# Performance work log

Hardware: AMD Instinct MI355X
Metric: run time of the kernel (lower is better)

## Reference

```python
import jax, jax.numpy as jnp
import numpy as np

B, L, D = 32, 256, 512
MAX_DUR = 8.0
MAX_LEN = int(L * MAX_DUR)  # static upper bound on expanded length (round(u<8) <= 8)


def setup_inputs() -> dict:
    key = jax.random.key(0)
    k1, k2 = jax.random.split(key)
    att_out = jax.random.normal(k1, (B, L, D), dtype=jnp.float32)
    # predicted per-phoneme durations in frames (float, gets rounded inside)
    duration = jax.random.uniform(k2, (B, L), dtype=jnp.float32, minval=0.0, maxval=MAX_DUR)
    return {"att_out": att_out, "duration": duration, "alpha": 1}


def reference(att_out, duration, alpha):
    # r[b,l] = number of times phoneme l is repeated (torch.round = half-to-even, same as jnp.round)
    r = jnp.round(duration * alpha).astype(jnp.int32)                 # [B, L]
    csum = jnp.cumsum(r, axis=1)                                      # [B, L] cumulative end offsets
    total = csum[:, -1]                                               # [B] valid length per batch
    pos = jnp.arange(MAX_LEN, dtype=jnp.int32)                        # [T]
    # output frame t comes from phoneme index = first l with csum[l] > t
    idx = jax.vmap(lambda c: jnp.searchsorted(c, pos, side='right'))(csum)  # [B, T]
    idx = jnp.minimum(idx, L - 1)
    out = jnp.take_along_axis(att_out, idx[:, :, None], axis=1)       # [B, T, D] gather-expand
    mask = (pos[None, :] < total[:, None])[:, :, None]                # zero-pad like pad_sequence
    return jnp.where(mask, out, jnp.zeros((), dtype=att_out.dtype))
```

## Files before the change

kernel.cpp:

```cpp
#include <hip/hip_runtime.h>


constexpr int B = 32;
constexpr int L = 256;
constexpr int D = 512;
constexpr int MAX_LEN = 2048;
constexpr int POS_PER_BLOCK = 16;
constexpr int THREADS = 256;

__global__ __launch_bounds__(THREADS) void length_regulator_kernel(
    const float* __restrict__ att_out,
    const float* __restrict__ duration,
    const int*   __restrict__ alpha_p,
    float*       __restrict__ out)
{
    __shared__ int csum[L];

    const int b        = blockIdx.y;
    const int pos_base = blockIdx.x * POS_PER_BLOCK;
    const int tid      = threadIdx.x;

    const float alpha = (float)alpha_p[0];

    int v = (int)rintf(duration[b * L + tid] * alpha);
    csum[tid] = v;
    __syncthreads();
    #pragma unroll
    for (int off = 1; off < L; off <<= 1) {
        int add = (tid >= off) ? csum[tid - off] : 0;
        __syncthreads();
        csum[tid] += add;
        __syncthreads();
    }
    const int total = csum[L - 1];

    const int lane_in_row = tid & 127;
    const int row_in_pass = tid >> 7;

    const float4* __restrict__ src4 = (const float4*)(att_out + (size_t)b * L * D);
    float4*       __restrict__ dst4 = (float4*)(out + (size_t)b * MAX_LEN * D);

    #pragma unroll
    for (int i = 0; i < POS_PER_BLOCK; i += 2) {
        const int p = pos_base + i + row_in_pass;
        float4 val;
        if (p < total) {
            int lo = 0, hi = L;
            #pragma unroll
            while (lo < hi) {
                int mid = (lo + hi) >> 1;
                if (csum[mid] <= p) lo = mid + 1; else hi = mid;
            }
            val = src4[(size_t)lo * (D / 4) + lane_in_row];
        } else {
            val = make_float4(0.f, 0.f, 0.f, 0.f);
        }
        dst4[(size_t)p * (D / 4) + lane_in_row] = val;
    }
}

extern "C" void kernel_launch(void* const* d_in, const int* in_sizes, int n_in,
                              void* d_out, int out_size, void* d_ws, size_t ws_size,
                              hipStream_t stream) {
    const float* att_out  = (const float*)d_in[0];
    const float* duration = (const float*)d_in[1];
    const int*   alpha    = (const int*)d_in[2];
    float*       out      = (float*)d_out;

    dim3 grid(MAX_LEN / POS_PER_BLOCK, B);
    dim3 block(THREADS);
    length_regulator_kernel<<<grid, block, 0, stream>>>(att_out, duration, alpha, out);
}
```

Baseline: 156.7 us.

## Use wave-shuffle scan, shared index table, and XCD-aware batch mapping

Replaces the shared-memory Hillis-Steele scan (many barriers) with a wavefront shuffle scan plus a cross-wave offset. Phoneme indices for the block's positions are found once into a shared table instead of every thread binary searching. Each block now covers 32 positions, and blocks are remapped so all blocks of one batch land on the same XCD, improving L2 reuse of att_out rows. Padded positions now load a clamped row and zero it, which adds some redundant reads.

```diff
diff --git a/kernel.cpp b/kernel.cpp
--- a/kernel.cpp
+++ b/kernel.cpp
@@ -5,7 +5,7 @@
 constexpr int L = 256;
 constexpr int D = 512;
 constexpr int MAX_LEN = 2048;
-constexpr int POS_PER_BLOCK = 16;
+constexpr int POS = 32;
 constexpr int THREADS = 256;
 
 __global__ __launch_bounds__(THREADS) void length_regulator_kernel(
@@ -15,47 +15,68 @@
     float*       __restrict__ out)
 {
     __shared__ int csum[L];
+    __shared__ int idx_tab[POS];
+    __shared__ int wsum[4];
 
-    const int b        = blockIdx.y;
-    const int pos_base = blockIdx.x * POS_PER_BLOCK;
-    const int tid      = threadIdx.x;
+    const int tid  = threadIdx.x;
+    const int lane = tid & 63;
+    const int wave = tid >> 6;
+
+    const int lin      = blockIdx.y * gridDim.x + blockIdx.x;
+    const int xcd      = lin & 7;
+    const int slot     = lin >> 3;
+    const int b        = xcd * (B / 8) + (slot >> 6);
+    const int pos_base = (slot & 63) * POS;
 
     const float alpha = (float)alpha_p[0];
 
     int v = (int)rintf(duration[b * L + tid] * alpha);
-    csum[tid] = v;
+    int x = v;
+    #pragma unroll
+    for (int off = 1; off < 64; off <<= 1) {
+        int y = __shfl_up(x, off);
+        x += (lane >= off) ? y : 0;
+    }
+    if (lane == 63) wsum[wave] = x;
     __syncthreads();
-    #pragma unroll
-    for (int off = 1; off < L; off <<= 1) {
-        int add = (tid >= off) ? csum[tid - off] : 0;
-        __syncthreads();
-        csum[tid] += add;
-        __syncthreads();
+    const int w0 = wsum[0], w1 = wsum[1], w2 = wsum[2], w3 = wsum[3];
+    const int total = w0 + w1 + w2 + w3;
+    const int woff = (wave > 0 ? w0 : 0) + (wave > 1 ? w1 : 0) + (wave > 2 ? w2 : 0);
+    csum[tid] = x + woff;
+    __syncthreads();
+
+    if (tid < POS) {
+        const int p = pos_base + tid;
+        int lo = 0;
+        #pragma unroll
+        for (int step = 128; step >= 1; step >>= 1) {
+            const int nxt = lo + step;
+            if (nxt <= L && csum[nxt - 1] <= p) lo = nxt;
+        }
+        idx_tab[tid] = min(lo, L - 1);
     }
-    const int total = csum[L - 1];
+    __syncthreads();
 
-    const int lane_in_row = tid & 127;
-    const int row_in_pass = tid >> 7;
+    const int lane_r = tid & 127;
+    const int rowsel = tid >> 7;
 
     const float4* __restrict__ src4 = (const float4*)(att_out + (size_t)b * L * D);
-    float4*       __restrict__ dst4 = (float4*)(out + (size_t)b * MAX_LEN * D);
+    float4*       __restrict__ dst4 =
+        (float4*)(out + ((size_t)b * MAX_LEN + pos_base) * D);
 
     #pragma unroll
-    for (int i = 0; i < POS_PER_BLOCK; i += 2) {
-        const int p = pos_base + i + row_in_pass;
+    for (int i = 0; i < POS; i += 2) {
+        const int rp = i + rowsel;
+        const int p  = pos_base + rp;
+        const int srow = idx_tab[rp];
+        float4 t = src4[(size_t)srow * (D / 4) + lane_r];
         float4 val;
-        if (p < total) {
-            int lo = 0, hi = L;
-            #pragma unroll
-            while (lo < hi) {
-                int mid = (lo + hi) >> 1;
-                if (csum[mid] <= p) lo = mid + 1; else hi = mid;
-            }
-            val = src4[(size_t)lo * (D / 4) + lane_in_row];
-        } else {
-            val = make_float4(0.f, 0.f, 0.f, 0.f);
-        }
-        dst4[(size_t)p * (D / 4) + lane_in_row] = val;
+        const bool keep = (p < total);
+        val.x = keep ? t.x : 0.f;
+        val.y = keep ? t.y : 0.f;
+        val.z = keep ? t.z : 0.f;
+        val.w = keep ? t.w : 0.f;
+        dst4[(size_t)rp * (D / 4) + lane_r] = val;
     }
 }
 
@@ -67,7 +88,7 @@
     const int*   alpha    = (const int*)d_in[2];
     float*       out      = (float*)d_out;
 
-    dim3 grid(MAX_LEN / POS_PER_BLOCK, B);
+    dim3 grid(MAX_LEN / POS, B);
     dim3 block(THREADS);
     length_regulator_kernel<<<grid, block, 0, stream>>>(att_out, duration, alpha, out);
 }
```

Measured after the change: 150.9 us. 3.7% less time.
